# Performance work log

Measured on AMD Instinct MI355X. Metric: run time of the kernel, lower is better.

The kernel has to match this reference:

```python
import jax, jax.numpy as jnp
import numpy as np

IN_FEATURES = 4096
OUT_FEATURES = 8192
LUT_SIZE = 65536  # 256 * 256 two-level codebook


def setup_inputs() -> dict:
    key = jax.random.key(0)
    k_x, k_b, k_f, k_s, k_l = jax.random.split(key, 5)
    x = jax.random.normal(k_x, (2, 256, IN_FEATURES), dtype=jnp.float32)
    base_idx = jax.random.randint(k_b, (OUT_FEATURES, IN_FEATURES), 0, 256, dtype=jnp.int32)
    fine_idx = jax.random.randint(k_f, (OUT_FEATURES, IN_FEATURES), 0, 256, dtype=jnp.int32)
    scale = jax.random.uniform(k_s, (OUT_FEATURES, 1), dtype=jnp.float32)
    lut = jax.random.normal(k_l, (LUT_SIZE,), dtype=jnp.float32)
    return {"x": x, "base_idx": base_idx, "fine_idx": fine_idx, "scale": scale, "lut": lut}


def reference(x, base_idx, fine_idx, scale, lut):
    # Two-level LUT dequant: combined 16-bit index = base*256 + fine
    combined_idx = base_idx * 256 + fine_idx              # [out, in] int32
    weights = lut[combined_idx] * scale                   # [out, in] fp32, per-row scale
    # F.linear(x, weights) == x @ weights.T
    return jnp.einsum('bsi,oi->bso', x, weights)
```

## Files before the change

### kernel.cpp

```cpp
#include <hip/hip_runtime.h>

typedef unsigned short ushort_t;
typedef unsigned int   uint32;
typedef __attribute__((ext_vector_type(8)))  short short8;
typedef __attribute__((ext_vector_type(4)))  float floatx4;
typedef __attribute__((ext_vector_type(16))) float floatx16;

#define IN_F   4096
#define OUT_F  8192
#define M_TOT  512

__device__ __forceinline__ ushort_t f2bf(float f) {
    uint32 u = __builtin_bit_cast(uint32, f);
    u += 0x7FFFu + ((u >> 16) & 1u);
    return (ushort_t)(u >> 16);
}
__device__ __forceinline__ uint32 pack2bf(float a, float b) {
    return (uint32)f2bf(a) | ((uint32)f2bf(b) << 16);
}

__global__ void cvt_x_kernel(const float* __restrict__ x, ushort_t* __restrict__ xb) {
    int i = (blockIdx.x * 256 + threadIdx.x) * 8;
    float4 v0 = *(const float4*)(x + i);
    float4 v1 = *(const float4*)(x + i + 4);
    short8 s;
    s[0] = (short)f2bf(v0.x); s[1] = (short)f2bf(v0.y);
    s[2] = (short)f2bf(v0.z); s[3] = (short)f2bf(v0.w);
    s[4] = (short)f2bf(v1.x); s[5] = (short)f2bf(v1.y);
    s[6] = (short)f2bf(v1.z); s[7] = (short)f2bf(v1.w);
    *(short8*)(xb + i) = s;
}

__global__ __launch_bounds__(1024, 4)
void dequant_kernel(const int* __restrict__ base_idx, const int* __restrict__ fine_idx,
                    const float* __restrict__ lut, ushort_t* __restrict__ wq)
{
    __shared__ ushort_t sh_lut[65536];
    const int tid = threadIdx.x;
    for (int i = tid * 4; i < 65536; i += 1024 * 4) {
        float4 v = *(const float4*)(lut + i);
        *(uint32*)&sh_lut[i]     = pack2bf(v.x, v.y);
        *(uint32*)&sh_lut[i + 2] = pack2bf(v.z, v.w);
    }

    const int row   = blockIdx.x * 32 + (tid >> 5);
    const int kbase = blockIdx.y * 2048 + (tid & 31) * 4;
    const int* bp = base_idx + (size_t)row * IN_F + kbase;
    const int* fp = fine_idx + (size_t)row * IN_F + kbase;
    ushort_t*  op = wq       + (size_t)row * IN_F + kbase;

    int4 cb[2][4], cf[2][4];
#pragma unroll
    for (int u = 0; u < 4; ++u) {
        cb[0][u] = *(const int4*)(bp + u * 128);
        cf[0][u] = *(const int4*)(fp + u * 128);
    }
#pragma unroll
    for (int u = 0; u < 4; ++u) {
        cb[1][u] = *(const int4*)(bp + (4 + u) * 128);
        cf[1][u] = *(const int4*)(fp + (4 + u) * 128);
    }
    __syncthreads();

#pragma unroll
    for (int b = 0; b < 4; ++b) {
        const int cur = b & 1;
#pragma unroll
        for (int u = 0; u < 4; ++u) {
            uint32 w0 = (uint32)sh_lut[(cb[cur][u].x << 8) + cf[cur][u].x]
                      | ((uint32)sh_lut[(cb[cur][u].y << 8) + cf[cur][u].y] << 16);
            uint32 w1 = (uint32)sh_lut[(cb[cur][u].z << 8) + cf[cur][u].z]
                      | ((uint32)sh_lut[(cb[cur][u].w << 8) + cf[cur][u].w] << 16);
            uint2 wv; wv.x = w0; wv.y = w1;
            *(uint2*)(op + (size_t)(b * 4 + u) * 128) = wv;
        }
        if (b + 2 < 4) {
#pragma unroll
            for (int u = 0; u < 4; ++u) {
                cb[cur][u] = *(const int4*)(bp + ((b + 2) * 4 + u) * 128);
                cf[cur][u] = *(const int4*)(fp + ((b + 2) * 4 + u) * 128);
            }
        }
    }
}

#define BK 128
__global__ __launch_bounds__(256)
void gemm_kernel(const ushort_t* __restrict__ xb, const ushort_t* __restrict__ wq,
                 const float* __restrict__ scale, float* __restrict__ out)
{
    __shared__ ushort_t shA[2][128 * BK];
    __shared__ ushort_t shB[2][128 * BK];

    const int tid  = threadIdx.x;
    const int wave = tid >> 6;
    const int m0   = blockIdx.x * 128;
    const int n0   = blockIdx.y * 128;

    const int g = (tid & 15) ^ ((tid >> 4) & 7);
    const ushort_t* aBase = xb + (size_t)(m0 + (tid >> 4)) * IN_F + g * 8;
    const ushort_t* bBase = wq + (size_t)(n0 + (tid >> 4)) * IN_F + g * 8;
    typedef __attribute__((address_space(3))) ushort_t lds_us;
    typedef const __attribute__((address_space(1))) void gvoid;
    lds_us* sA3 = (lds_us*)&shA[0][0];
    lds_us* sB3 = (lds_us*)&shB[0][0];

    const int lane = tid & 63;
    const int l31  = lane & 31;
    const int lhi  = lane >> 5;
    const int qm   = wave & 1;
    const int qn   = wave >> 1;
    const int rx   = l31 & 7;

    floatx16 acc[2][2];
    const floatx16 z16 = {0.f,0.f,0.f,0.f,0.f,0.f,0.f,0.f,0.f,0.f,0.f,0.f,0.f,0.f,0.f,0.f};
    acc[0][0] = z16; acc[0][1] = z16; acc[1][0] = z16; acc[1][1] = z16;

#pragma unroll
    for (int i = 0; i < 8; ++i) {
        __builtin_amdgcn_global_load_lds((gvoid*)(aBase + (size_t)i * 16 * IN_F),
            (__attribute__((address_space(3))) void*)(sA3 + i * 2048 + wave * 512), 16, 0, 0);
        __builtin_amdgcn_global_load_lds((gvoid*)(bBase + (size_t)i * 16 * IN_F),
            (__attribute__((address_space(3))) void*)(sB3 + i * 2048 + wave * 512), 16, 0, 0);
    }

    const int NIT = IN_F / BK;
    for (int t = 0; t < NIT; ++t) {
        __syncthreads();

        if (t + 1 < NIT) {
            const int buf = (t + 1) & 1;
            const size_t kb = (size_t)(t + 1) * BK;
#pragma unroll
            for (int i = 0; i < 8; ++i) {
                __builtin_amdgcn_global_load_lds((gvoid*)(aBase + (size_t)i * 16 * IN_F + kb),
                    (__attribute__((address_space(3))) void*)(sA3 + buf * 128 * BK + i * 2048 + wave * 512),
                    16, 0, 0);
                __builtin_amdgcn_global_load_lds((gvoid*)(bBase + (size_t)i * 16 * IN_F + kb),
                    (__attribute__((address_space(3))) void*)(sB3 + buf * 128 * BK + i * 2048 + wave * 512),
                    16, 0, 0);
            }
        }

        const ushort_t* wA = shA[t & 1];
        const ushort_t* wB = shB[t & 1];
#pragma unroll
        for (int ks = 0; ks < 8; ++ks) {
            const int p = ((2 * ks + lhi) ^ rx) * 8;
            short8 a0 = *(const short8*)&wA[(qm * 64 +      l31) * BK + p];
            short8 a1 = *(const short8*)&wA[(qm * 64 + 32 + l31) * BK + p];
            short8 b0 = *(const short8*)&wB[(qn * 64 +      l31) * BK + p];
            short8 b1 = *(const short8*)&wB[(qn * 64 + 32 + l31) * BK + p];
            acc[0][0] = __builtin_amdgcn_mfma_f32_32x32x16_bf16(a0, b0, acc[0][0], 0, 0, 0);
            acc[0][1] = __builtin_amdgcn_mfma_f32_32x32x16_bf16(a0, b1, acc[0][1], 0, 0, 0);
            acc[1][0] = __builtin_amdgcn_mfma_f32_32x32x16_bf16(a1, b0, acc[1][0], 0, 0, 0);
            acc[1][1] = __builtin_amdgcn_mfma_f32_32x32x16_bf16(a1, b1, acc[1][1], 0, 0, 0);
        }
    }

#pragma unroll
    for (int nt = 0; nt < 2; ++nt) {
        const int col = n0 + qn * 64 + nt * 32 + l31;
        const float sc = scale[col];
#pragma unroll
        for (int mt = 0; mt < 2; ++mt) {
            const int rbase = m0 + qm * 64 + mt * 32 + 4 * lhi;
#pragma unroll
            for (int reg = 0; reg < 16; ++reg) {
                const int row = rbase + (reg & 3) + 8 * (reg >> 2);
                out[(size_t)row * OUT_F + col] = acc[mt][nt][reg] * sc;
            }
        }
    }
}

#define NB  32
#define FBK 128
#define WS  136
#define NITER (IN_F / FBK)
template<bool XBF16>
__global__ __launch_bounds__(1024, 4)
void ghost_kernel(const float* __restrict__ xf, const ushort_t* __restrict__ xb,
                  const int* __restrict__ base_idx, const int* __restrict__ fine_idx,
                  const float* __restrict__ scale, const float* __restrict__ lut,
                  float* __restrict__ out)
{
    __shared__ ushort_t sh_lut[65536];
    __shared__ ushort_t sh_w[2][NB * WS];
    const int tid = threadIdx.x;
    const int n0  = blockIdx.x * NB;
    for (int i = tid * 4; i < 65536; i += 1024 * 4) {
        float4 v = *(const float4*)(lut + i);
        sh_lut[i + 0] = f2bf(v.x); sh_lut[i + 1] = f2bf(v.y);
        sh_lut[i + 2] = f2bf(v.z); sh_lut[i + 3] = f2bf(v.w);
    }
    const int sn  = tid >> 5;
    const int skq = (tid & 31) * 4;
    const int* bp = base_idx + (size_t)(n0 + sn) * IN_F + skq;
    const int* fp = fine_idx + (size_t)(n0 + sn) * IN_F + skq;
    __syncthreads();
    int4 pb = *(const int4*)(bp);
    int4 pf = *(const int4*)(fp);
    {
        uint32 w0 = (uint32)sh_lut[(pb.x << 8) + pf.x] | ((uint32)sh_lut[(pb.y << 8) + pf.y] << 16);
        uint32 w1 = (uint32)sh_lut[(pb.z << 8) + pf.z] | ((uint32)sh_lut[(pb.w << 8) + pf.w] << 16);
        uint2 wv; wv.x = w0; wv.y = w1;
        *(uint2*)&sh_w[0][sn * WS + skq] = wv;
    }
    pb = *(const int4*)(bp + FBK);
    pf = *(const int4*)(fp + FBK);
    __syncthreads();
    const int lane = tid & 63;
    const int wave = tid >> 6;
    const int l16  = lane & 15;
    const int quad = lane >> 4;
    floatx4 acc[2][2];
    const floatx4 zero = {0.f, 0.f, 0.f, 0.f};
    acc[0][0] = zero; acc[0][1] = zero; acc[1][0] = zero; acc[1][1] = zero;
    const int mrow = wave * 32 + l16;
    const ushort_t* xrow  = XBF16 ? (xb + (size_t)mrow * IN_F + quad * 8) : (const ushort_t*)nullptr;
    const float*    xrowf = XBF16 ? (const float*)nullptr : (xf + (size_t)mrow * IN_F + quad * 8);
    for (int t = 0; t < NITER; ++t) {
        const int k0 = t * FBK;
        {
            uint32 w0 = (uint32)sh_lut[(pb.x << 8) + pf.x] | ((uint32)sh_lut[(pb.y << 8) + pf.y] << 16);
            uint32 w1 = (uint32)sh_lut[(pb.z << 8) + pf.z] | ((uint32)sh_lut[(pb.w << 8) + pf.w] << 16);
            uint2 wv; wv.x = w0; wv.y = w1;
            *(uint2*)&sh_w[(t + 1) & 1][sn * WS + skq] = wv;
        }
        {
            const int kk = (t + 2 < NITER ? t + 2 : NITER - 1) * FBK;
            pb = *(const int4*)(bp + kk);
            pf = *(const int4*)(fp + kk);
        }
        const ushort_t* wb = sh_w[t & 1];
#pragma unroll
        for (int ks = 0; ks < 4; ++ks) {
            const int kk = k0 + ks * 32;
            short8 b0 = *(const short8*)&wb[l16        * WS + ks * 32 + quad * 8];
            short8 b1 = *(const short8*)&wb[(16 + l16) * WS + ks * 32 + quad * 8];
            short8 a0, a1;
            if (XBF16) {
                a0 = *(const short8*)(xrow + kk);
                a1 = *(const short8*)(xrow + (size_t)16 * IN_F + kk);
            } else {
                const float* p0 = xrowf + kk;
                const float* p1 = xrowf + (size_t)16 * IN_F + kk;
                float4 u0 = *(const float4*)p0, u1 = *(const float4*)(p0 + 4);
                float4 v0 = *(const float4*)p1, v1 = *(const float4*)(p1 + 4);
                a0[0] = (short)f2bf(u0.x); a0[1] = (short)f2bf(u0.y);
                a0[2] = (short)f2bf(u0.z); a0[3] = (short)f2bf(u0.w);
                a0[4] = (short)f2bf(u1.x); a0[5] = (short)f2bf(u1.y);
                a0[6] = (short)f2bf(u1.z); a0[7] = (short)f2bf(u1.w);
                a1[0] = (short)f2bf(v0.x); a1[1] = (short)f2bf(v0.y);
                a1[2] = (short)f2bf(v0.z); a1[3] = (short)f2bf(v0.w);
                a1[4] = (short)f2bf(v1.x); a1[5] = (short)f2bf(v1.y);
                a1[6] = (short)f2bf(v1.z); a1[7] = (short)f2bf(v1.w);
            }
            acc[0][0] = __builtin_amdgcn_mfma_f32_16x16x32_bf16(a0, b0, acc[0][0], 0, 0, 0);
            acc[0][1] = __builtin_amdgcn_mfma_f32_16x16x32_bf16(a0, b1, acc[0][1], 0, 0, 0);
            acc[1][0] = __builtin_amdgcn_mfma_f32_16x16x32_bf16(a1, b0, acc[1][0], 0, 0, 0);
            acc[1][1] = __builtin_amdgcn_mfma_f32_16x16x32_bf16(a1, b1, acc[1][1], 0, 0, 0);
        }
        __syncthreads();
    }
#pragma unroll
    for (int nf = 0; nf < 2; ++nf) {
        const int col = n0 + nf * 16 + l16;
        const float sc = scale[col];
#pragma unroll
        for (int f = 0; f < 2; ++f) {
            const int r0 = wave * 32 + f * 16 + quad * 4;
#pragma unroll
            for (int r = 0; r < 4; ++r) {
                out[(size_t)(r0 + r) * OUT_F + col] = acc[f][nf][r] * sc;
            }
        }
    }
}

extern "C" void kernel_launch(void* const* d_in, const int* in_sizes, int n_in,
                              void* d_out, int out_size, void* d_ws, size_t ws_size,
                              hipStream_t stream) {
    const float* x      = (const float*)d_in[0];
    const int*   bidx   = (const int*)d_in[1];
    const int*   fidx   = (const int*)d_in[2];
    const float* scale  = (const float*)d_in[3];
    const float* lut    = (const float*)d_in[4];
    float*       out    = (float*)d_out;

    const size_t xb_bytes = (size_t)M_TOT * IN_F * sizeof(ushort_t);
    const size_t wq_bytes = (size_t)OUT_F * IN_F * sizeof(ushort_t);

    if (ws_size >= xb_bytes + wq_bytes) {
        ushort_t* xbuf = (ushort_t*)d_ws;
        ushort_t* wbuf = (ushort_t*)((char*)d_ws + xb_bytes);
        cvt_x_kernel<<<1024, 256, 0, stream>>>(x, xbuf);
        dequant_kernel<<<dim3(256, 2), 1024, 0, stream>>>(bidx, fidx, lut, wbuf);
        gemm_kernel<<<dim3(4, 64), 256, 0, stream>>>(xbuf, wbuf, scale, out);
    } else if (ws_size >= xb_bytes) {
        ushort_t* xbuf = (ushort_t*)d_ws;
        cvt_x_kernel<<<1024, 256, 0, stream>>>(x, xbuf);
        ghost_kernel<true><<<OUT_F / NB, 1024, 0, stream>>>(x, xbuf, bidx, fidx, scale, lut, out);
    } else {
        ghost_kernel<false><<<OUT_F / NB, 1024, 0, stream>>>(x, nullptr, bidx, fidx, scale, lut, out);
    }
}
```

Baseline: 387.9 us.

## Split GEMM over K into two partial passes with a separate reduce kernel

Adds a split-K GEMM path that runs two K halves as separate blocks (grid z=2) writing fp32 partials, then a reduce kernel sums them and applies the per-row scale. It drops LDS double-buffering in favour of single-buffered tiles with two barriers per step, aiming for two blocks per CU. The fallback GEMM is also changed to single buffering. The goal is more blocks (512 instead of 256) to fill the CUs. The cost is 32 MB of extra partial writes and reads, one more launch, and lost load/compute overlap within each block.

```diff
diff --git a/kernel.cpp b/kernel.cpp
--- a/kernel.cpp
+++ b/kernel.cpp
@@ -85,25 +85,26 @@
 }
 
 #define BK 128
-__global__ __launch_bounds__(256)
-void gemm_kernel(const ushort_t* __restrict__ xb, const ushort_t* __restrict__ wq,
-                 const float* __restrict__ scale, float* __restrict__ out)
-{
-    __shared__ ushort_t shA[2][128 * BK];
-    __shared__ ushort_t shB[2][128 * BK];
+__global__ __launch_bounds__(256, 2)
+void gemm_split_kernel(const ushort_t* __restrict__ xb, const ushort_t* __restrict__ wq,
+                       float* __restrict__ part)
+{
+    __shared__ ushort_t shA[128 * BK];
+    __shared__ ushort_t shB[128 * BK];
 
     const int tid  = threadIdx.x;
     const int wave = tid >> 6;
     const int m0   = blockIdx.x * 128;
     const int n0   = blockIdx.y * 128;
+    const int kz   = blockIdx.z * (IN_F / 2);
 
     const int g = (tid & 15) ^ ((tid >> 4) & 7);
-    const ushort_t* aBase = xb + (size_t)(m0 + (tid >> 4)) * IN_F + g * 8;
-    const ushort_t* bBase = wq + (size_t)(n0 + (tid >> 4)) * IN_F + g * 8;
+    const ushort_t* aBase = xb + (size_t)(m0 + (tid >> 4)) * IN_F + kz + g * 8;
+    const ushort_t* bBase = wq + (size_t)(n0 + (tid >> 4)) * IN_F + kz + g * 8;
     typedef __attribute__((address_space(3))) ushort_t lds_us;
     typedef const __attribute__((address_space(1))) void gvoid;
-    lds_us* sA3 = (lds_us*)&shA[0][0];
-    lds_us* sB3 = (lds_us*)&shB[0][0];
+    lds_us* sA3 = (lds_us*)shA;
+    lds_us* sB3 = (lds_us*)shB;
 
     const int lane = tid & 63;
     const int l31  = lane & 31;
@@ -116,48 +117,118 @@
     const floatx16 z16 = {0.f,0.f,0.f,0.f,0.f,0.f,0.f,0.f,0.f,0.f,0.f,0.f,0.f,0.f,0.f,0.f};
     acc[0][0] = z16; acc[0][1] = z16; acc[1][0] = z16; acc[1][1] = z16;
 
-#pragma unroll
-    for (int i = 0; i < 8; ++i) {
-        __builtin_amdgcn_global_load_lds((gvoid*)(aBase + (size_t)i * 16 * IN_F),
-            (__attribute__((address_space(3))) void*)(sA3 + i * 2048 + wave * 512), 16, 0, 0);
-        __builtin_amdgcn_global_load_lds((gvoid*)(bBase + (size_t)i * 16 * IN_F),
-            (__attribute__((address_space(3))) void*)(sB3 + i * 2048 + wave * 512), 16, 0, 0);
-    }
-
-    const int NIT = IN_F / BK;
-    for (int t = 0; t < NIT; ++t) {
-        __syncthreads();
-
-        if (t + 1 < NIT) {
-            const int buf = (t + 1) & 1;
-            const size_t kb = (size_t)(t + 1) * BK;
-#pragma unroll
-            for (int i = 0; i < 8; ++i) {
-                __builtin_amdgcn_global_load_lds((gvoid*)(aBase + (size_t)i * 16 * IN_F + kb),
-                    (__attribute__((address_space(3))) void*)(sA3 + buf * 128 * BK + i * 2048 + wave * 512),
-                    16, 0, 0);
-                __builtin_amdgcn_global_load_lds((gvoid*)(bBase + (size_t)i * 16 * IN_F + kb),
-                    (__attribute__((address_space(3))) void*)(sB3 + buf * 128 * BK + i * 2048 + wave * 512),
-                    16, 0, 0);
-            }
-        }
-
-        const ushort_t* wA = shA[t & 1];
-        const ushort_t* wB = shB[t & 1];
+    for (int kb = 0; kb < IN_F / 2; kb += BK) {
+#pragma unroll
+        for (int i = 0; i < 8; ++i) {
+            __builtin_amdgcn_global_load_lds((gvoid*)(aBase + (size_t)i * 16 * IN_F + kb),
+                (__attribute__((address_space(3))) void*)(sA3 + i * 2048 + wave * 512),
+                16, 0, 0);
+            __builtin_amdgcn_global_load_lds((gvoid*)(bBase + (size_t)i * 16 * IN_F + kb),
+                (__attribute__((address_space(3))) void*)(sB3 + i * 2048 + wave * 512),
+                16, 0, 0);
+        }
+        __syncthreads();
+
 #pragma unroll
         for (int ks = 0; ks < 8; ++ks) {
             const int p = ((2 * ks + lhi) ^ rx) * 8;
-            short8 a0 = *(const short8*)&wA[(qm * 64 +      l31) * BK + p];
-            short8 a1 = *(const short8*)&wA[(qm * 64 + 32 + l31) * BK + p];
-            short8 b0 = *(const short8*)&wB[(qn * 64 +      l31) * BK + p];
-            short8 b1 = *(const short8*)&wB[(qn * 64 + 32 + l31) * BK + p];
+            short8 a0 = *(const short8*)&shA[(qm * 64 +      l31) * BK + p];
+            short8 a1 = *(const short8*)&shA[(qm * 64 + 32 + l31) * BK + p];
+            short8 b0 = *(const short8*)&shB[(qn * 64 +      l31) * BK + p];
+            short8 b1 = *(const short8*)&shB[(qn * 64 + 32 + l31) * BK + p];
             acc[0][0] = __builtin_amdgcn_mfma_f32_32x32x16_bf16(a0, b0, acc[0][0], 0, 0, 0);
             acc[0][1] = __builtin_amdgcn_mfma_f32_32x32x16_bf16(a0, b1, acc[0][1], 0, 0, 0);
             acc[1][0] = __builtin_amdgcn_mfma_f32_32x32x16_bf16(a1, b0, acc[1][0], 0, 0, 0);
             acc[1][1] = __builtin_amdgcn_mfma_f32_32x32x16_bf16(a1, b1, acc[1][1], 0, 0, 0);
         }
-    }
-
+        __syncthreads();
+    }
+
+    float* pz = part + (size_t)blockIdx.z * M_TOT * OUT_F;
+#pragma unroll
+    for (int nt = 0; nt < 2; ++nt) {
+        const int col = n0 + qn * 64 + nt * 32 + l31;
+#pragma unroll
+        for (int mt = 0; mt < 2; ++mt) {
+            const int rbase = m0 + qm * 64 + mt * 32 + 4 * lhi;
+#pragma unroll
+            for (int reg = 0; reg < 16; ++reg) {
+                const int row = rbase + (reg & 3) + 8 * (reg >> 2);
+                pz[(size_t)row * OUT_F + col] = acc[mt][nt][reg];
+            }
+        }
+    }
+}
+
+__global__ void reduce_kernel(const float* __restrict__ p0, const float* __restrict__ p1,
+                              const float* __restrict__ scale, float* __restrict__ out)
+{
+    const int i = (blockIdx.x * 256 + threadIdx.x) * 4;
+    float4 a = *(const float4*)(p0 + i);
+    float4 b = *(const float4*)(p1 + i);
+    float4 s = *(const float4*)(scale + (i & (OUT_F - 1)));
+    float4 r;
+    r.x = (a.x + b.x) * s.x;
+    r.y = (a.y + b.y) * s.y;
+    r.z = (a.z + b.z) * s.z;
+    r.w = (a.w + b.w) * s.w;
+    *(float4*)(out + i) = r;
+}
+
+__global__ __launch_bounds__(256)
+void gemm_full_kernel(const ushort_t* __restrict__ xb, const ushort_t* __restrict__ wq,
+                      const float* __restrict__ scale, float* __restrict__ out)
+{
+    __shared__ ushort_t shA[128 * BK];
+    __shared__ ushort_t shB[128 * BK];
+
+    const int tid  = threadIdx.x;
+    const int wave = tid >> 6;
+    const int m0   = blockIdx.x * 128;
+    const int n0   = blockIdx.y * 128;
+
+    const int g = (tid & 15) ^ ((tid >> 4) & 7);
+    const ushort_t* aBase = xb + (size_t)(m0 + (tid >> 4)) * IN_F + g * 8;
+    const ushort_t* bBase = wq + (size_t)(n0 + (tid >> 4)) * IN_F + g * 8;
+    typedef __attribute__((address_space(3))) ushort_t lds_us;
+    typedef const __attribute__((address_space(1))) void gvoid;
+    lds_us* sA3 = (lds_us*)shA;
+    lds_us* sB3 = (lds_us*)shB;
+
+    const int lane = tid & 63;
+    const int l31  = lane & 31;
+    const int lhi  = lane >> 5;
+    const int qm   = wave & 1;
+    const int qn   = wave >> 1;
+    const int rx   = l31 & 7;
+
+    floatx16 acc[2][2];
+    const floatx16 z16 = {0.f,0.f,0.f,0.f,0.f,0.f,0.f,0.f,0.f,0.f,0.f,0.f,0.f,0.f,0.f,0.f};
+    acc[0][0] = z16; acc[0][1] = z16; acc[1][0] = z16; acc[1][1] = z16;
+
+    for (int kb = 0; kb < IN_F; kb += BK) {
+#pragma unroll
+        for (int i = 0; i < 8; ++i) {
+            __builtin_amdgcn_global_load_lds((gvoid*)(aBase + (size_t)i * 16 * IN_F + kb),
+                (__attribute__((address_space(3))) void*)(sA3 + i * 2048 + wave * 512), 16, 0, 0);
+            __builtin_amdgcn_global_load_lds((gvoid*)(bBase + (size_t)i * 16 * IN_F + kb),
+                (__attribute__((address_space(3))) void*)(sB3 + i * 2048 + wave * 512), 16, 0, 0);
+        }
+        __syncthreads();
+#pragma unroll
+        for (int ks = 0; ks < 8; ++ks) {
+            const int p = ((2 * ks + lhi) ^ rx) * 8;
+            short8 a0 = *(const short8*)&shA[(qm * 64 +      l31) * BK + p];
+            short8 a1 = *(const short8*)&shA[(qm * 64 + 32 + l31) * BK + p];
+            short8 b0 = *(const short8*)&shB[(qn * 64 +      l31) * BK + p];
+            short8 b1 = *(const short8*)&shB[(qn * 64 + 32 + l31) * BK + p];
+            acc[0][0] = __builtin_amdgcn_mfma_f32_32x32x16_bf16(a0, b0, acc[0][0], 0, 0, 0);
+            acc[0][1] = __builtin_amdgcn_mfma_f32_32x32x16_bf16(a0, b1, acc[0][1], 0, 0, 0);
+            acc[1][0] = __builtin_amdgcn_mfma_f32_32x32x16_bf16(a1, b0, acc[1][0], 0, 0, 0);
+            acc[1][1] = __builtin_amdgcn_mfma_f32_32x32x16_bf16(a1, b1, acc[1][1], 0, 0, 0);
+        }
+        __syncthreads();
+    }
 #pragma unroll
     for (int nt = 0; nt < 2; ++nt) {
         const int col = n0 + qn * 64 + nt * 32 + l31;
@@ -291,13 +362,23 @@
 
     const size_t xb_bytes = (size_t)M_TOT * IN_F * sizeof(ushort_t);
     const size_t wq_bytes = (size_t)OUT_F * IN_F * sizeof(ushort_t);
-
-    if (ws_size >= xb_bytes + wq_bytes) {
+    const size_t pt_bytes = (size_t)M_TOT * OUT_F * sizeof(float);
+
+    if (ws_size >= xb_bytes + wq_bytes + 2 * pt_bytes) {
+        ushort_t* xbuf = (ushort_t*)d_ws;
+        ushort_t* wbuf = (ushort_t*)((char*)d_ws + xb_bytes);
+        float*    part = (float*)((char*)d_ws + xb_bytes + wq_bytes);
+        cvt_x_kernel<<<1024, 256, 0, stream>>>(x, xbuf);
+        dequant_kernel<<<dim3(256, 2), 1024, 0, stream>>>(bidx, fidx, lut, wbuf);
+        gemm_split_kernel<<<dim3(4, 64, 2), 256, 0, stream>>>(xbuf, wbuf, part);
+        reduce_kernel<<<(M_TOT * OUT_F) / (256 * 4), 256, 0, stream>>>(
+            part, part + (size_t)M_TOT * OUT_F, scale, out);
+    } else if (ws_size >= xb_bytes + wq_bytes) {
         ushort_t* xbuf = (ushort_t*)d_ws;
         ushort_t* wbuf = (ushort_t*)((char*)d_ws + xb_bytes);
         cvt_x_kernel<<<1024, 256, 0, stream>>>(x, xbuf);
         dequant_kernel<<<dim3(256, 2), 1024, 0, stream>>>(bidx, fidx, lut, wbuf);
-        gemm_kernel<<<dim3(4, 64), 256, 0, stream>>>(xbuf, wbuf, scale, out);
+        gemm_full_kernel<<<dim3(4, 64), 256, 0, stream>>>(xbuf, wbuf, scale, out);
     } else if (ws_size >= xb_bytes) {
         ushort_t* xbuf = (ushort_t*)d_ws;
         cvt_x_kernel<<<1024, 256, 0, stream>>>(x, xbuf);
```

Measured after the change: 364.7 us. 1.06x faster.
